# Performance work log

Hardware: AMD Instinct MI355X
Metric: run time of the kernel (lower is better)

The kernel has to match this reference:

```python
import jax, jax.numpy as jnp
import numpy as np

EMBED_DIM = 1024
NUM_HEADS = 16
HEAD_DIM = EMBED_DIM // NUM_HEADS
THRESHOLD = 0.001
B, S = 8, 1024


def setup_inputs() -> dict:
    key = jax.random.key(0)
    ks = jax.random.split(key, 7)
    sc = 1.0 / np.sqrt(EMBED_DIM)
    return {
        "x": jax.random.normal(ks[0], (B, S, EMBED_DIM), dtype=jnp.float32),
        "Wq": jax.random.normal(ks[1], (NUM_HEADS, EMBED_DIM, HEAD_DIM), dtype=jnp.float32) * sc,
        "bq": jax.random.normal(ks[2], (NUM_HEADS, HEAD_DIM), dtype=jnp.float32) * 0.01,
        "Wk": jax.random.normal(ks[3], (NUM_HEADS, EMBED_DIM, HEAD_DIM), dtype=jnp.float32) * sc,
        "bk": jax.random.normal(ks[4], (NUM_HEADS, HEAD_DIM), dtype=jnp.float32) * 0.01,
        "Wv": jax.random.normal(ks[5], (NUM_HEADS, EMBED_DIM, HEAD_DIM), dtype=jnp.float32) * sc,
        "bv": jax.random.normal(ks[6], (NUM_HEADS, HEAD_DIM), dtype=jnp.float32) * 0.01,
    }


def thresholded_softmax(scores, threshold):
    # softmax over last dim, zero entries below threshold, renormalize
    s = jax.nn.softmax(scores, axis=-1)
    s = jnp.where(s < threshold, 0.0, s)
    return s / (jnp.sum(s, axis=-1, keepdims=True) + 1e-12)


def reference(x, Wq, bq, Wk, bk, Wv, bv):
    # x: [B,S,D]; Wq/Wk/Wv: [H,D,e]; biases: [H,e]
    scale = jnp.asarray(EMBED_DIM ** 0.5, x.dtype)  # note: scales by sqrt(embed_dim), not head_dim
    Q = jnp.einsum("bsd,hde->hbse", x, Wq) + bq[:, None, None, :]
    K = jnp.einsum("bsd,hde->hbse", x, Wk) + bk[:, None, None, :]
    V = jnp.einsum("bsd,hde->hbse", x, Wv) + bv[:, None, None, :]
    scores = jnp.einsum("hbse,hbte->hbst", Q, K) / scale  # [H,B,S,S]
    att = thresholded_softmax(scores, THRESHOLD)
    latent = jnp.einsum("hbst,hbte->hbse", att, V)  # [H,B,S,e]
    # concat heads along last dim in head order -> [B,S,H*e]
    residual = jnp.transpose(latent, (1, 2, 0, 3)).reshape(x.shape[0], x.shape[1], -1)
    x_res = x + residual  # dropout p=0.0 -> identity
    return (x_res, att)
```

## Files before the change

### kernel.cpp

```cpp
#include <hip/hip_runtime.h>
#include <hip/hip_bf16.h>
#include <cstdint>
#include <cstddef>

#define B_ 8
#define S_ 1024
#define H_ 16
#define E_ 64
#define D_ 1024

typedef unsigned short u16;
typedef short s16x8 __attribute__((ext_vector_type(8)));
typedef float f32x4 __attribute__((ext_vector_type(4)));

__device__ __forceinline__ u16 f2b(float f) {
  union { float f; unsigned u; } v; v.f = f;
  unsigned u = v.u;
  return (u16)((u + 0x7FFFu + ((u >> 16) & 1u)) >> 16);
}

__device__ __forceinline__ void gload16(const void* g, void* lds) {
  __builtin_amdgcn_global_load_lds(
      (const __attribute__((address_space(1))) void*)g,
      (__attribute__((address_space(3))) void*)lds, 16, 0, 0);
}

#define BARL() do {                                          \
  asm volatile("s_waitcnt lgkmcnt(0)" ::: "memory");         \
  __builtin_amdgcn_sched_barrier(0);                         \
  __builtin_amdgcn_s_barrier();                              \
  __builtin_amdgcn_sched_barrier(0);                         \
  asm volatile("" ::: "memory");                             \
} while (0)

__global__ void k_prep(const float* __restrict__ x, u16* __restrict__ xb,
                       const float* __restrict__ Wq, const float* __restrict__ Wk,
                       const float* __restrict__ Wv, u16* __restrict__ wbt) {
  if (blockIdx.x < 4096) {
    size_t i = ((size_t)blockIdx.x * 256 + threadIdx.x) * 8;
    float4 a = *(const float4*)(x + i);
    float4 b = *(const float4*)(x + i + 4);
    uint4 o;
    o.x = f2b(a.x) | ((unsigned)f2b(a.y) << 16);
    o.y = f2b(a.z) | ((unsigned)f2b(a.w) << 16);
    o.z = f2b(b.x) | ((unsigned)f2b(b.y) << 16);
    o.w = f2b(b.z) | ((unsigned)f2b(b.w) << 16);
    *(uint4*)(xb + i) = o;
    return;
  }
  __shared__ u16 T[64][65];
  int bid = blockIdx.x - 4096;
  int d0 = (bid & 15) * 64;
  int mh = bid >> 4;
  int mat = mh >> 4, h = mh & 15;
  const float* W = (mat == 0) ? Wq : (mat == 1) ? Wk : Wv;
  int tid = threadIdx.x;
#pragma unroll
  for (int rep = 0; rep < 4; rep++) {
    int dl = rep * 16 + (tid >> 4);
    int e0 = (tid & 15) * 4;
    float4 v = *(const float4*)(W + (size_t)h * (D_ * E_) + (size_t)(d0 + dl) * E_ + e0);
    T[dl][e0] = f2b(v.x); T[dl][e0 + 1] = f2b(v.y);
    T[dl][e0 + 2] = f2b(v.z); T[dl][e0 + 3] = f2b(v.w);
  }
  __syncthreads();
#pragma unroll
  for (int rep = 0; rep < 4; rep++) {
    int el = rep * 16 + (tid >> 4);
    int dl0 = (tid & 15) * 4;
    ushort4 o;
    o.x = T[dl0][el]; o.y = T[dl0 + 1][el]; o.z = T[dl0 + 2][el]; o.w = T[dl0 + 3][el];
    int n = mat * 1024 + h * 64 + el;
    *(ushort4*)(wbt + (size_t)n * D_ + d0 + dl0) = o;
  }
}

__global__ __launch_bounds__(256) void k_qkv(
    const u16* __restrict__ xb, const u16* __restrict__ wbt,
    const float* __restrict__ bq, const float* __restrict__ bk, const float* __restrict__ bv,
    u16* __restrict__ Qb, u16* __restrict__ Kb, u16* __restrict__ Vt) {
  __shared__ u16 As[128 * 64];
  __shared__ u16 Bs[128 * 64];
  int tid = threadIdx.x, l = tid & 63, w = tid >> 6;
  int bid = blockIdx.x;
  int xcd = bid & 7, i = bid >> 3;
  int m0 = (xcd * 8 + i / 24) * 128;
  int n0 = (i % 24) * 128;
  int wm = w >> 1, wn = w & 1;
  int rl = l & 15, kg = l >> 4;
  f32x4 acc[4][4] = {};
  for (int k0 = 0; k0 < D_; k0 += 64) {
#pragma unroll
    for (int i2 = 0; i2 < 4; i2++) {
      int ci = w * 4 + i2;
      int r = ci * 8 + (l >> 3);
      int c = (l & 7) ^ (r & 7);
      gload16(xb  + (size_t)(m0 + r) * D_ + k0 + c * 8, (char*)As + ci * 1024);
      gload16(wbt + (size_t)(n0 + r) * D_ + k0 + c * 8, (char*)Bs + ci * 1024);
    }
    __syncthreads();
#pragma unroll
    for (int kk = 0; kk < 2; kk++) {
      s16x8 af[4], bfr[4];
      int chunk = kk * 4 + kg;
#pragma unroll
      for (int fm = 0; fm < 4; fm++) {
        int r = wm * 64 + fm * 16 + rl;
        af[fm] = *(const s16x8*)(As + r * 64 + ((chunk ^ (r & 7)) * 8));
      }
#pragma unroll
      for (int fn = 0; fn < 4; fn++) {
        int r = wn * 64 + fn * 16 + rl;
        bfr[fn] = *(const s16x8*)(Bs + r * 64 + ((chunk ^ (r & 7)) * 8));
      }
#pragma unroll
      for (int fm = 0; fm < 4; fm++)
#pragma unroll
        for (int fn = 0; fn < 4; fn++)
          acc[fm][fn] = __builtin_amdgcn_mfma_f32_16x16x32_bf16(af[fm], bfr[fn], acc[fm][fn], 0, 0, 0);
    }
    __syncthreads();
  }
#pragma unroll
  for (int fn = 0; fn < 4; fn++) {
    int n = n0 + wn * 64 + fn * 16 + rl;
    int mat = n >> 10, h = (n >> 6) & 15, e = n & 63;
    const float* bias = (mat == 0) ? bq : (mat == 1) ? bk : bv;
    float bval = bias[h * 64 + e];
    if (mat == 2) {
#pragma unroll
      for (int fm = 0; fm < 4; fm++) {
        int sq = m0 + wm * 64 + fm * 16 + kg * 4;
        int bb = sq >> 10, s = sq & 1023;
        ushort4 o;
        o.x = f2b(acc[fm][fn][0] + bval);
        o.y = f2b(acc[fm][fn][1] + bval);
        o.z = f2b(acc[fm][fn][2] + bval);
        o.w = f2b(acc[fm][fn][3] + bval);
        *(ushort4*)(Vt + ((size_t)((h * B_ + bb) * E_ + e) << 10) + s) = o;
      }
    } else {
      u16* dst = (mat == 0) ? Qb : Kb;
#pragma unroll
      for (int fm = 0; fm < 4; fm++)
#pragma unroll
        for (int j = 0; j < 4; j++) {
          int m = m0 + wm * 64 + fm * 16 + kg * 4 + j;
          int bb = m >> 10, s = m & 1023;
          dst[(size_t)((h * B_ + bb) * S_ + s) * E_ + e] = f2b(acc[fm][fn][j] + bval);
        }
    }
  }
}

__global__ __launch_bounds__(512, 2) void f_attn(
    const u16* __restrict__ Qb, const u16* __restrict__ Kb, const u16* __restrict__ Vt,
    const float* __restrict__ x, float* __restrict__ att, float* __restrict__ out) {
  __shared__ u16 Qlds[64 * 64];
  __shared__ u16 KV[1024 * 64];
  __shared__ u16 Ab[2][64 * 64];
  __shared__ float red[3][64][4];

  int p = blockIdx.x;
  int L = (p & 7) * 256 + (p >> 3);
  int hb = L >> 4, mblk = L & 15;
  int m0 = mblk * 64;
  int tid = threadIdx.x, l = tid & 63, w = tid >> 6;
  int rl = l & 15, kg = l >> 4;
  int rh = w >> 2, cq = w & 3;

  const u16* Qp = Qb + (size_t)hb * (S_ * E_) + (size_t)m0 * E_;
  const u16* Kp = Kb + (size_t)hb * (S_ * E_);
  const u16* Vp = Vt + (size_t)hb * (S_ * E_);

  {
    int r = w * 8 + (l >> 3), c = (l & 7) ^ (r & 7);
    gload16(Qp + (size_t)r * E_ + c * 8, (char*)Qlds + w * 1024);
  }
#pragma unroll
  for (int i = 0; i < 16; i++) {
    int ci = w * 16 + i;
    int r = ci * 8 + (l >> 3), c = (l & 7) ^ (r & 7);
    gload16(Kp + (size_t)r * E_ + c * 8, (char*)KV + ci * 1024);
  }
  __syncthreads();

  s16x8 af[2][2];
#pragma unroll
  for (int fm = 0; fm < 2; fm++)
#pragma unroll
    for (int kk = 0; kk < 2; kk++) {
      int r = rh * 32 + fm * 16 + rl, ch = kk * 4 + kg;
      af[fm][kk] = *(const s16x8*)((const char*)Qlds + r * 128 + ((ch ^ (r & 7)) * 16));
    }

  f32x4 acc[2][16];
#pragma unroll
  for (int fm = 0; fm < 2; fm++)
#pragma unroll
    for (int ct = 0; ct < 16; ct++)
#pragma unroll
      for (int j = 0; j < 4; j++) acc[fm][ct][j] = 0.f;

#pragma unroll
  for (int ct = 0; ct < 16; ct++) {
    s16x8 bf[2];
#pragma unroll
    for (int kk = 0; kk < 2; kk++) {
      int r = ct * 64 + cq * 16 + rl, ch = kk * 4 + kg;
      bf[kk] = *(const s16x8*)((const char*)KV + r * 128 + ((ch ^ (r & 7)) * 16));
    }
#pragma unroll
    for (int fm = 0; fm < 2; fm++)
#pragma unroll
      for (int kk = 0; kk < 2; kk++)
        acc[fm][ct] = __builtin_amdgcn_mfma_f32_16x16x32_bf16(af[fm][kk], bf[kk], acc[fm][ct], 0, 0, 0);
  }
  __syncthreads();

#pragma unroll
  for (int i = 0; i < 16; i++) {
    int ci = w * 16 + i;
    int e = ci >> 1, hf = ci & 1;
    int c = ((hf * 64 + l) & ~7) | ((l & 7) ^ (e & 7));
    gload16(Vp + (size_t)e * S_ + c * 8, (char*)KV + e * 2048 + hf * 1024);
  }

  float mx[2][4], Z[2][4], Z2[2][4];
#pragma unroll
  for (int fm = 0; fm < 2; fm++)
#pragma unroll
    for (int j = 0; j < 4; j++) {
      float m = acc[fm][0][j];
#pragma unroll
      for (int ct = 1; ct < 16; ct++) m = fmaxf(m, acc[fm][ct][j]);
#pragma unroll
      for (int off = 8; off >= 1; off >>= 1) m = fmaxf(m, __shfl_xor(m, off));
      mx[fm][j] = m;
    }
  if (rl == 0) {
#pragma unroll
    for (int fm = 0; fm < 2; fm++)
#pragma unroll
      for (int j = 0; j < 4; j++) red[0][rh * 32 + fm * 16 + kg * 4 + j][cq] = mx[fm][j];
  }
  BARL();
#pragma unroll
  for (int fm = 0; fm < 2; fm++)
#pragma unroll
    for (int j = 0; j < 4; j++) {
      f32x4 r4 = *(const f32x4*)&red[0][rh * 32 + fm * 16 + kg * 4 + j][0];
      mx[fm][j] = fmaxf(fmaxf(r4[0], r4[1]), fmaxf(r4[2], r4[3]));
    }
#pragma unroll
  for (int fm = 0; fm < 2; fm++)
#pragma unroll
    for (int j = 0; j < 4; j++) {
      float s = 0.f;
#pragma unroll
      for (int ct = 0; ct < 16; ct++) {
        float e = __expf((acc[fm][ct][j] - mx[fm][j]) * 0.03125f);
        acc[fm][ct][j] = e;
        s += e;
      }
#pragma unroll
      for (int off = 8; off >= 1; off >>= 1) s += __shfl_xor(s, off);
      Z[fm][j] = s;
    }
  if (rl == 0) {
#pragma unroll
    for (int fm = 0; fm < 2; fm++)
#pragma unroll
      for (int j = 0; j < 4; j++) red[1][rh * 32 + fm * 16 + kg * 4 + j][cq] = Z[fm][j];
  }
  BARL();
#pragma unroll
  for (int fm = 0; fm < 2; fm++)
#pragma unroll
    for (int j = 0; j < 4; j++) {
      f32x4 r4 = *(const f32x4*)&red[1][rh * 32 + fm * 16 + kg * 4 + j][0];
      Z[fm][j] = r4[0] + r4[1] + r4[2] + r4[3];
    }
#pragma unroll
  for (int fm = 0; fm < 2; fm++)
#pragma unroll
    for (int j = 0; j < 4; j++) {
      float thr = 0.001f * Z[fm][j];
      float s = 0.f;
#pragma unroll
      for (int ct = 0; ct < 16; ct++) {
        float e = acc[fm][ct][j];
        e = (e >= thr) ? e : 0.f;
        acc[fm][ct][j] = e;
        s += e;
      }
#pragma unroll
      for (int off = 8; off >= 1; off >>= 1) s += __shfl_xor(s, off);
      Z2[fm][j] = s;
    }
  if (rl == 0) {
#pragma unroll
    for (int fm = 0; fm < 2; fm++)
#pragma unroll
      for (int j = 0; j < 4; j++) red[2][rh * 32 + fm * 16 + kg * 4 + j][cq] = Z2[fm][j];
  }
  BARL();
#pragma unroll
  for (int fm = 0; fm < 2; fm++)
#pragma unroll
    for (int j = 0; j < 4; j++) {
      f32x4 r4 = *(const f32x4*)&red[2][rh * 32 + fm * 16 + kg * 4 + j][0];
      float z2 = r4[0] + r4[1] + r4[2] + r4[3];
      float inv = 1.f / (z2 + 1e-12f * Z[fm][j]);
#pragma unroll
      for (int ct = 0; ct < 16; ct++) acc[fm][ct][j] *= inv;
    }

  asm volatile("s_waitcnt vmcnt(0)" ::: "memory");
  __builtin_amdgcn_sched_barrier(0);

  float* attp = att + ((size_t)hb << 20) + ((size_t)m0 << 10);
#pragma unroll
  for (int fm = 0; fm < 2; fm++)
#pragma unroll
    for (int j = 0; j < 4; j++) {
      int m = rh * 32 + fm * 16 + kg * 4 + j;
#pragma unroll
      for (int ct = 0; ct < 16; ct++)
        attp[((size_t)m << 10) + ct * 64 + cq * 16 + rl] = acc[fm][ct][j];
    }

  int mh2 = w >> 1, nh2 = w & 1;
  f32x4 acc2[2];
#pragma unroll
  for (int fn = 0; fn < 2; fn++)
#pragma unroll
    for (int j = 0; j < 4; j++) acc2[fn][j] = 0.f;

#pragma unroll
  for (int fm = 0; fm < 2; fm++)
#pragma unroll
    for (int j = 0; j < 4; j++) {
      int m = rh * 32 + fm * 16 + kg * 4 + j;
      int tl = cq * 16 + rl;
      *(u16*)((char*)Ab[0] + m * 128 + (((tl >> 3) ^ (m & 7)) * 16) + (tl & 7) * 2)
          = f2b(acc[fm][0][j]);
    }
  BARL();

#pragma unroll
  for (int ct = 0; ct < 16; ct++) {
    s16x8 a2[2], b2[2][2];
#pragma unroll
    for (int kk = 0; kk < 2; kk++) {
      int ch = kk * 4 + kg;
      int rA = mh2 * 16 + rl;
      a2[kk] = *(const s16x8*)((const char*)Ab[ct & 1] + rA * 128 + ((ch ^ (rA & 7)) * 16));
#pragma unroll
      for (int fn = 0; fn < 2; fn++) {
        int e = nh2 * 32 + fn * 16 + rl;
        b2[fn][kk] = *(const s16x8*)((const char*)KV + e * 2048 + ct * 128 + ((ch ^ (e & 7)) * 16));
      }
    }
    if (ct < 15) {
#pragma unroll
      for (int fm = 0; fm < 2; fm++)
#pragma unroll
        for (int j = 0; j < 4; j++) {
          int m = rh * 32 + fm * 16 + kg * 4 + j;
          int tl = cq * 16 + rl;
          *(u16*)((char*)Ab[(ct + 1) & 1] + m * 128 + (((tl >> 3) ^ (m & 7)) * 16) + (tl & 7) * 2)
              = f2b(acc[fm][ct + 1][j]);
        }
    }
    __builtin_amdgcn_s_setprio(1);
#pragma unroll
    for (int fn = 0; fn < 2; fn++)
#pragma unroll
      for (int kk = 0; kk < 2; kk++)
        acc2[fn] = __builtin_amdgcn_mfma_f32_16x16x32_bf16(a2[kk], b2[fn][kk], acc2[fn], 0, 0, 0);
    __builtin_amdgcn_s_setprio(0);
    BARL();
  }

  int h = hb >> 3, bb = hb & 7;
#pragma unroll
  for (int fn = 0; fn < 2; fn++)
#pragma unroll
    for (int j = 0; j < 4; j++) {
      int m = m0 + mh2 * 16 + kg * 4 + j;
      int e = h * 64 + nh2 * 32 + fn * 16 + rl;
      size_t idx = (((size_t)bb * S_ + m) << 10) + e;
      out[idx] = x[idx] + acc2[fn][j];
    }
}

extern "C" void kernel_launch(void* const* d_in, const int* in_sizes, int n_in,
                              void* d_out, int out_size, void* d_ws, size_t ws_size,
                              hipStream_t stream) {
  const float* x  = (const float*)d_in[0];
  const float* Wq = (const float*)d_in[1];
  const float* bq = (const float*)d_in[2];
  const float* Wk = (const float*)d_in[3];
  const float* bk = (const float*)d_in[4];
  const float* Wv = (const float*)d_in[5];
  const float* bv = (const float*)d_in[6];
  float* xres = (float*)d_out;
  float* att  = xres + (size_t)B_ * S_ * D_;

  char* ws = (char*)d_ws;
  u16* xb  = (u16*)(ws);
  u16* wbt = (u16*)(ws + 16777216);
  u16* Qb  = (u16*)(ws + 23068672);
  u16* Kb  = (u16*)(ws + 39845888);
  u16* Vt  = (u16*)(ws + 56623104);

  k_prep  <<<dim3(4864), dim3(256), 0, stream>>>(x, xb, Wq, Wk, Wv, wbt);
  k_qkv   <<<dim3(1536), dim3(256), 0, stream>>>(xb, wbt, bq, bk, bv, Qb, Kb, Vt);
  f_attn  <<<dim3(2048), dim3(512), 0, stream>>>(Qb, Kb, Vt, x, att, xres);
}
```

Measured before the change: 296.7 us.

## Stream K and V through double-buffered LDS chunks with smaller 32-row attention blocks

The attention kernel now uses 32 query rows per block and 256 threads instead of 64 rows and 512 threads, and it stops holding the whole K or V tile in LDS. K and V are streamed in 128-key chunks through a double buffer, with the next chunk's async load issued while MFMAs run on the current one. The attention-matrix stores are interleaved with the PV loop, and the x residual is prefetched early. This shrinks LDS per block so more blocks can be resident and hides load latency. The cost is twice as many blocks, each re-reading K and V, plus extra barriers per chunk.

Result: slower. 447.9 us (+51.0%).

```diff
diff --git a/kernel.cpp b/kernel.cpp
--- a/kernel.cpp
+++ b/kernel.cpp
@@ -153,21 +153,20 @@
   }
 }
 
-__global__ __launch_bounds__(512, 2) void f_attn(
+__global__ __launch_bounds__(256) void f_attn(
     const u16* __restrict__ Qb, const u16* __restrict__ Kb, const u16* __restrict__ Vt,
     const float* __restrict__ x, float* __restrict__ att, float* __restrict__ out) {
-  __shared__ u16 Qlds[64 * 64];
-  __shared__ u16 KV[1024 * 64];
-  __shared__ u16 Ab[2][64 * 64];
-  __shared__ float red[3][64][4];
+  __shared__ u16 Kc[2][128 * 64];
+  __shared__ u16 Ab[2][32 * 128];
+  __shared__ u16 Qlds[32 * 64];
+  __shared__ float red[3][32][4];
 
   int p = blockIdx.x;
-  int L = (p & 7) * 256 + (p >> 3);
-  int hb = L >> 4, mblk = L & 15;
-  int m0 = mblk * 64;
+  int L = (p & 7) * 512 + (p >> 3);
+  int hb = L >> 5, mblk = L & 31;
+  int m0 = mblk * 32;
   int tid = threadIdx.x, l = tid & 63, w = tid >> 6;
   int rl = l & 15, kg = l >> 4;
-  int rh = w >> 2, cq = w & 3;
 
   const u16* Qp = Qb + (size_t)hb * (S_ * E_) + (size_t)m0 * E_;
   const u16* Kp = Kb + (size_t)hb * (S_ * E_);
@@ -178,10 +177,10 @@
     gload16(Qp + (size_t)r * E_ + c * 8, (char*)Qlds + w * 1024);
   }
 #pragma unroll
-  for (int i = 0; i < 16; i++) {
-    int ci = w * 16 + i;
+  for (int i = 0; i < 4; i++) {
+    int ci = w * 4 + i;
     int r = ci * 8 + (l >> 3), c = (l & 7) ^ (r & 7);
-    gload16(Kp + (size_t)r * E_ + c * 8, (char*)KV + ci * 1024);
+    gload16(Kp + (size_t)r * E_ + c * 8, (char*)Kc[0] + ci * 1024);
   }
   __syncthreads();
 
@@ -190,41 +189,66 @@
   for (int fm = 0; fm < 2; fm++)
 #pragma unroll
     for (int kk = 0; kk < 2; kk++) {
-      int r = rh * 32 + fm * 16 + rl, ch = kk * 4 + kg;
-      af[fm][kk] = *(const s16x8*)((const char*)Qlds + r * 128 + ((ch ^ (r & 7)) * 16));
+      int q = fm * 16 + rl, ch = kk * 4 + kg;
+      af[fm][kk] = *(const s16x8*)((const char*)Qlds + q * 128 + ((ch ^ (q & 7)) * 16));
     }
 
   f32x4 acc[2][16];
 #pragma unroll
   for (int fm = 0; fm < 2; fm++)
 #pragma unroll
-    for (int ct = 0; ct < 16; ct++)
-#pragma unroll
-      for (int j = 0; j < 4; j++) acc[fm][ct][j] = 0.f;
-
-#pragma unroll
-  for (int ct = 0; ct < 16; ct++) {
-    s16x8 bf[2];
-#pragma unroll
-    for (int kk = 0; kk < 2; kk++) {
-      int r = ct * 64 + cq * 16 + rl, ch = kk * 4 + kg;
-      bf[kk] = *(const s16x8*)((const char*)KV + r * 128 + ((ch ^ (r & 7)) * 16));
-    }
+    for (int tc = 0; tc < 16; tc++)
+#pragma unroll
+      for (int j = 0; j < 4; j++) acc[fm][tc][j] = 0.f;
+
+#pragma unroll
+  for (int c = 0; c < 8; c++) {
+    if (c < 7) {
+#pragma unroll
+      for (int i = 0; i < 4; i++) {
+        int ci = w * 4 + i;
+        int r = ci * 8 + (l >> 3), cc = (l & 7) ^ (r & 7);
+        gload16(Kp + (size_t)((c + 1) * 128 + r) * E_ + cc * 8,
+                (char*)Kc[(c + 1) & 1] + ci * 1024);
+      }
+    }
+    s16x8 bf[2][2];
+#pragma unroll
+    for (int fn = 0; fn < 2; fn++)
+#pragma unroll
+      for (int kk = 0; kk < 2; kk++) {
+        int r = w * 32 + fn * 16 + rl, ch = kk * 4 + kg;
+        bf[fn][kk] = *(const s16x8*)((const char*)Kc[c & 1] + r * 128 + ((ch ^ (r & 7)) * 16));
+      }
 #pragma unroll
     for (int fm = 0; fm < 2; fm++)
 #pragma unroll
-      for (int kk = 0; kk < 2; kk++)
-        acc[fm][ct] = __builtin_amdgcn_mfma_f32_16x16x32_bf16(af[fm][kk], bf[kk], acc[fm][ct], 0, 0, 0);
-  }
-  __syncthreads();
-
-#pragma unroll
-  for (int i = 0; i < 16; i++) {
-    int ci = w * 16 + i;
-    int e = ci >> 1, hf = ci & 1;
-    int c = ((hf * 64 + l) & ~7) | ((l & 7) ^ (e & 7));
-    gload16(Vp + (size_t)e * S_ + c * 8, (char*)KV + e * 2048 + hf * 1024);
-  }
+      for (int fn = 0; fn < 2; fn++)
+#pragma unroll
+        for (int kk = 0; kk < 2; kk++)
+          acc[fm][c * 2 + fn] = __builtin_amdgcn_mfma_f32_16x16x32_bf16(
+              af[fm][kk], bf[fn][kk], acc[fm][c * 2 + fn], 0, 0, 0);
+    __syncthreads();
+  }
+
+#pragma unroll
+  for (int i = 0; i < 4; i++) {
+    int ci = w * 4 + i;
+    int e = ci * 4 + (l >> 4);
+    int s = l & 15;
+    int cl = (s & 8) | ((s & 7) ^ (e & 7));
+    gload16(Vp + (size_t)e * S_ + cl * 8, (char*)Kc[0] + ci * 1024);
+  }
+  int h = hb >> 3, bb = hb & 7;
+  float xv[2][4];
+#pragma unroll
+  for (int fm = 0; fm < 2; fm++)
+#pragma unroll
+    for (int j = 0; j < 4; j++) {
+      int q = m0 + fm * 16 + kg * 4 + j;
+      int e = h * 64 + w * 16 + rl;
+      xv[fm][j] = x[(((size_t)bb * S_ + q) << 10) + e];
+    }
 
   float mx[2][4], Z[2][4], Z2[2][4];
 #pragma unroll
@@ -233,7 +257,7 @@
     for (int j = 0; j < 4; j++) {
       float m = acc[fm][0][j];
 #pragma unroll
-      for (int ct = 1; ct < 16; ct++) m = fmaxf(m, acc[fm][ct][j]);
+      for (int tc = 1; tc < 16; tc++) m = fmaxf(m, acc[fm][tc][j]);
 #pragma unroll
       for (int off = 8; off >= 1; off >>= 1) m = fmaxf(m, __shfl_xor(m, off));
       mx[fm][j] = m;
@@ -242,14 +266,14 @@
 #pragma unroll
     for (int fm = 0; fm < 2; fm++)
 #pragma unroll
-      for (int j = 0; j < 4; j++) red[0][rh * 32 + fm * 16 + kg * 4 + j][cq] = mx[fm][j];
+      for (int j = 0; j < 4; j++) red[0][fm * 16 + kg * 4 + j][w] = mx[fm][j];
   }
   BARL();
 #pragma unroll
   for (int fm = 0; fm < 2; fm++)
 #pragma unroll
     for (int j = 0; j < 4; j++) {
-      f32x4 r4 = *(const f32x4*)&red[0][rh * 32 + fm * 16 + kg * 4 + j][0];
+      f32x4 r4 = *(const f32x4*)&red[0][fm * 16 + kg * 4 + j][0];
       mx[fm][j] = fmaxf(fmaxf(r4[0], r4[1]), fmaxf(r4[2], r4[3]));
     }
 #pragma unroll
@@ -258,9 +282,9 @@
     for (int j = 0; j < 4; j++) {
       float s = 0.f;
 #pragma unroll
-      for (int ct = 0; ct < 16; ct++) {
-        float e = __expf((acc[fm][ct][j] - mx[fm][j]) * 0.03125f);
-        acc[fm][ct][j] = e;
+      for (int tc = 0; tc < 16; tc++) {
+        float e = __expf((acc[fm][tc][j] - mx[fm][j]) * 0.03125f);
+        acc[fm][tc][j] = e;
         s += e;
       }
 #pragma unroll
@@ -271,14 +295,14 @@
 #pragma unroll
     for (int fm = 0; fm < 2; fm++)
 #pragma unroll
-      for (int j = 0; j < 4; j++) red[1][rh * 32 + fm * 16 + kg * 4 + j][cq] = Z[fm][j];
+      for (int j = 0; j < 4; j++) red[1][fm * 16 + kg * 4 + j][w] = Z[fm][j];
   }
   BARL();
 #pragma unroll
   for (int fm = 0; fm < 2; fm++)
 #pragma unroll
     for (int j = 0; j < 4; j++) {
-      f32x4 r4 = *(const f32x4*)&red[1][rh * 32 + fm * 16 + kg * 4 + j][0];
+      f32x4 r4 = *(const f32x4*)&red[1][fm * 16 + kg * 4 + j][0];
       Z[fm][j] = r4[0] + r4[1] + r4[2] + r4[3];
     }
 #pragma unroll
@@ -288,10 +312,10 @@
       float thr = 0.001f * Z[fm][j];
       float s = 0.f;
 #pragma unroll
-      for (int ct = 0; ct < 16; ct++) {
-        float e = acc[fm][ct][j];
+      for (int tc = 0; tc < 16; tc++) {
+        float e = acc[fm][tc][j];
         e = (e >= thr) ? e : 0.f;
-        acc[fm][ct][j] = e;
+        acc[fm][tc][j] = e;
         s += e;
       }
 #pragma unroll
@@ -302,96 +326,101 @@
 #pragma unroll
     for (int fm = 0; fm < 2; fm++)
 #pragma unroll
-      for (int j = 0; j < 4; j++) red[2][rh * 32 + fm * 16 + kg * 4 + j][cq] = Z2[fm][j];
+      for (int j = 0; j < 4; j++) red[2][fm * 16 + kg * 4 + j][w] = Z2[fm][j];
   }
   BARL();
 #pragma unroll
   for (int fm = 0; fm < 2; fm++)
 #pragma unroll
     for (int j = 0; j < 4; j++) {
-      f32x4 r4 = *(const f32x4*)&red[2][rh * 32 + fm * 16 + kg * 4 + j][0];
+      f32x4 r4 = *(const f32x4*)&red[2][fm * 16 + kg * 4 + j][0];
       float z2 = r4[0] + r4[1] + r4[2] + r4[3];
       float inv = 1.f / (z2 + 1e-12f * Z[fm][j]);
 #pragma unroll
-      for (int ct = 0; ct < 16; ct++) acc[fm][ct][j] *= inv;
-    }
-
-  asm volatile("s_waitcnt vmcnt(0)" ::: "memory");
-  __builtin_amdgcn_sched_barrier(0);
-
+      for (int tc = 0; tc < 16; tc++) acc[fm][tc][j] *= inv;
+    }
+
+#pragma unroll
+  for (int fm = 0; fm < 2; fm++)
+#pragma unroll
+    for (int fn = 0; fn < 2; fn++)
+#pragma unroll
+      for (int j = 0; j < 4; j++) {
+        int q = fm * 16 + kg * 4 + j;
+        int tl = w * 32 + fn * 16 + rl;
+        int chk = tl >> 3;
+        int sw = (chk & 8) | ((chk & 7) ^ (q & 7));
+        *(u16*)((char*)Ab[0] + q * 256 + sw * 16 + (tl & 7) * 2) = f2b(acc[fm][fn][j]);
+      }
+  __syncthreads();
+
+  f32x4 acc2[2] = {};
   float* attp = att + ((size_t)hb << 20) + ((size_t)m0 << 10);
 #pragma unroll
-  for (int fm = 0; fm < 2; fm++)
-#pragma unroll
-    for (int j = 0; j < 4; j++) {
-      int m = rh * 32 + fm * 16 + kg * 4 + j;
-#pragma unroll
-      for (int ct = 0; ct < 16; ct++)
-        attp[((size_t)m << 10) + ct * 64 + cq * 16 + rl] = acc[fm][ct][j];
-    }
-
-  int mh2 = w >> 1, nh2 = w & 1;
-  f32x4 acc2[2];
-#pragma unroll
-  for (int fn = 0; fn < 2; fn++)
-#pragma unroll
-    for (int j = 0; j < 4; j++) acc2[fn][j] = 0.f;
-
-#pragma unroll
-  for (int fm = 0; fm < 2; fm++)
-#pragma unroll
-    for (int j = 0; j < 4; j++) {
-      int m = rh * 32 + fm * 16 + kg * 4 + j;
-      int tl = cq * 16 + rl;
-      *(u16*)((char*)Ab[0] + m * 128 + (((tl >> 3) ^ (m & 7)) * 16) + (tl & 7) * 2)
-          = f2b(acc[fm][0][j]);
-    }
-  BARL();
-
-#pragma unroll
-  for (int ct = 0; ct < 16; ct++) {
-    s16x8 a2[2], b2[2][2];
-#pragma unroll
-    for (int kk = 0; kk < 2; kk++) {
-      int ch = kk * 4 + kg;
-      int rA = mh2 * 16 + rl;
-      a2[kk] = *(const s16x8*)((const char*)Ab[ct & 1] + rA * 128 + ((ch ^ (rA & 7)) * 16));
-#pragma unroll
-      for (int fn = 0; fn < 2; fn++) {
-        int e = nh2 * 32 + fn * 16 + rl;
-        b2[fn][kk] = *(const s16x8*)((const char*)KV + e * 2048 + ct * 128 + ((ch ^ (e & 7)) * 16));
-      }
-    }
-    if (ct < 15) {
+  for (int c = 0; c < 8; c++) {
+    if (c < 7) {
+#pragma unroll
+      for (int i = 0; i < 4; i++) {
+        int ci = w * 4 + i;
+        int e = ci * 4 + (l >> 4);
+        int s = l & 15;
+        int cl = (s & 8) | ((s & 7) ^ (e & 7));
+        gload16(Vp + (size_t)e * S_ + (c + 1) * 128 + cl * 8,
+                (char*)Kc[(c + 1) & 1] + ci * 1024);
+      }
 #pragma unroll
       for (int fm = 0; fm < 2; fm++)
 #pragma unroll
+        for (int fn = 0; fn < 2; fn++)
+#pragma unroll
+          for (int j = 0; j < 4; j++) {
+            int q = fm * 16 + kg * 4 + j;
+            int tl = w * 32 + fn * 16 + rl;
+            int chk = tl >> 3;
+            int sw = (chk & 8) | ((chk & 7) ^ (q & 7));
+            *(u16*)((char*)Ab[(c + 1) & 1] + q * 256 + sw * 16 + (tl & 7) * 2)
+                = f2b(acc[fm][(c + 1) * 2 + fn][j]);
+          }
+    }
+#pragma unroll
+    for (int ks = 0; ks < 4; ks++) {
+      int chk = ks * 4 + kg;
+      s16x8 a2[2], b2;
+#pragma unroll
+      for (int fm = 0; fm < 2; fm++) {
+        int q = fm * 16 + rl;
+        int sw = (chk & 8) | ((chk & 7) ^ (q & 7));
+        a2[fm] = *(const s16x8*)((const char*)Ab[c & 1] + q * 256 + sw * 16);
+      }
+      {
+        int e = w * 16 + rl;
+        int sw = (chk & 8) | ((chk & 7) ^ (e & 7));
+        b2 = *(const s16x8*)((const char*)Kc[c & 1] + e * 256 + sw * 16);
+      }
+#pragma unroll
+      for (int fm = 0; fm < 2; fm++)
+        acc2[fm] = __builtin_amdgcn_mfma_f32_16x16x32_bf16(a2[fm], b2, acc2[fm], 0, 0, 0);
+    }
+#pragma unroll
+    for (int fm = 0; fm < 2; fm++)
+#pragma unroll
+      for (int fn = 0; fn < 2; fn++)
+#pragma unroll
         for (int j = 0; j < 4; j++) {
-          int m = rh * 32 + fm * 16 + kg * 4 + j;
-          int tl = cq * 16 + rl;
-          *(u16*)((char*)Ab[(ct + 1) & 1] + m * 128 + (((tl >> 3) ^ (m & 7)) * 16) + (tl & 7) * 2)
-              = f2b(acc[fm][ct + 1][j]);
+          int q = fm * 16 + kg * 4 + j;
+          int t = c * 128 + w * 32 + fn * 16 + rl;
+          attp[((size_t)q << 10) + t] = acc[fm][c * 2 + fn][j];
         }
-    }
-    __builtin_amdgcn_s_setprio(1);
-#pragma unroll
-    for (int fn = 0; fn < 2; fn++)
-#pragma unroll
-      for (int kk = 0; kk < 2; kk++)
-        acc2[fn] = __builtin_amdgcn_mfma_f32_16x16x32_bf16(a2[kk], b2[fn][kk], acc2[fn], 0, 0, 0);
-    __builtin_amdgcn_s_setprio(0);
-    BARL();
-  }
-
-  int h = hb >> 3, bb = hb & 7;
-#pragma unroll
-  for (int fn = 0; fn < 2; fn++)
-#pragma unroll
-    for (int j = 0; j < 4; j++) {
-      int m = m0 + mh2 * 16 + kg * 4 + j;
-      int e = h * 64 + nh2 * 32 + fn * 16 + rl;
-      size_t idx = (((size_t)bb * S_ + m) << 10) + e;
-      out[idx] = x[idx] + acc2[fn][j];
+    __syncthreads();
+  }
+
+#pragma unroll
+  for (int fm = 0; fm < 2; fm++)
+#pragma unroll
+    for (int j = 0; j < 4; j++) {
+      int q = m0 + fm * 16 + kg * 4 + j;
+      int e = h * 64 + w * 16 + rl;
+      out[(((size_t)bb * S_ + q) << 10) + e] = xv[fm][j] + acc2[fm][j];
     }
 }
 
@@ -417,5 +446,5 @@
 
   k_prep  <<<dim3(4864), dim3(256), 0, stream>>>(x, xb, Wq, Wk, Wv, wbt);
   k_qkv   <<<dim3(1536), dim3(256), 0, stream>>>(xb, wbt, bq, bk, bv, Qb, Kb, Vt);
-  f_attn  <<<dim3(2048), dim3(512), 0, stream>>>(Qb, Kb, Vt, x, att, xres);
-}
+  f_attn  <<<dim3(4096), dim3(256), 0, stream>>>(Qb, Kb, Vt, x, att, xres);
+}
```

## Transpose QK^T MFMA so each lane owns a query row, vectorize att stores

Applied to the files above, without the earlier changes.

The score MFMA is computed as K·Q^T so each lane holds one query row across 32 key tiles. Row max and sum reductions then need only two cross-lane shuffles instead of four per row. The attention matrix is stored with float4 writes instead of scalar writes. The P tiles for the PV matmul are packed with v_cvt_pk_bf16_f32 into 8-byte LDS stores. The aim is to cut reduction shuffles and store instruction count on a kernel dominated by writing the large att output, with a new LDS reduction layout and P-tile write pattern.

Result: slower. 316.5 us (+6.6%).

```diff
diff --git a/kernel.cpp b/kernel.cpp
--- a/kernel.cpp
+++ b/kernel.cpp
@@ -17,6 +17,12 @@
   union { float f; unsigned u; } v; v.f = f;
   unsigned u = v.u;
   return (u16)((u + 0x7FFFu + ((u >> 16) & 1u)) >> 16);
+}
+
+__device__ __forceinline__ unsigned cvtpk(float a, float b) {
+  unsigned r;
+  asm("v_cvt_pk_bf16_f32 %0, %1, %2" : "=v"(r) : "v"(a), "v"(b));
+  return r;
 }
 
 __device__ __forceinline__ void gload16(const void* g, void* lds) {
@@ -159,7 +165,7 @@
   __shared__ u16 Qlds[64 * 64];
   __shared__ u16 KV[1024 * 64];
   __shared__ u16 Ab[2][64 * 64];
-  __shared__ float red[3][64][4];
+  __shared__ float red[3][4][16][2];
 
   int p = blockIdx.x;
   int L = (p & 7) * 256 + (p >> 3);
@@ -167,7 +173,8 @@
   int m0 = mblk * 64;
   int tid = threadIdx.x, l = tid & 63, w = tid >> 6;
   int rl = l & 15, kg = l >> 4;
-  int rh = w >> 2, cq = w & 3;
+  int qg = w >> 1, pr = w & 1;
+  int q = qg * 16 + rl;
 
   const u16* Qp = Qb + (size_t)hb * (S_ * E_) + (size_t)m0 * E_;
   const u16* Kp = Kb + (size_t)hb * (S_ * E_);
@@ -185,36 +192,23 @@
   }
   __syncthreads();
 
-  s16x8 af[2][2];
-#pragma unroll
-  for (int fm = 0; fm < 2; fm++)
-#pragma unroll
-    for (int kk = 0; kk < 2; kk++) {
-      int r = rh * 32 + fm * 16 + rl, ch = kk * 4 + kg;
-      af[fm][kk] = *(const s16x8*)((const char*)Qlds + r * 128 + ((ch ^ (r & 7)) * 16));
-    }
-
-  f32x4 acc[2][16];
-#pragma unroll
-  for (int fm = 0; fm < 2; fm++)
-#pragma unroll
-    for (int ct = 0; ct < 16; ct++)
-#pragma unroll
-      for (int j = 0; j < 4; j++) acc[fm][ct][j] = 0.f;
-
-#pragma unroll
-  for (int ct = 0; ct < 16; ct++) {
-    s16x8 bf[2];
-#pragma unroll
-    for (int kk = 0; kk < 2; kk++) {
-      int r = ct * 64 + cq * 16 + rl, ch = kk * 4 + kg;
-      bf[kk] = *(const s16x8*)((const char*)KV + r * 128 + ((ch ^ (r & 7)) * 16));
-    }
-#pragma unroll
-    for (int fm = 0; fm < 2; fm++)
-#pragma unroll
-      for (int kk = 0; kk < 2; kk++)
-        acc[fm][ct] = __builtin_amdgcn_mfma_f32_16x16x32_bf16(af[fm][kk], bf[kk], acc[fm][ct], 0, 0, 0);
+  s16x8 qf[2];
+#pragma unroll
+  for (int kk = 0; kk < 2; kk++)
+    qf[kk] = *(const s16x8*)((const char*)Qlds + q * 128 + (((kk * 4 + kg) ^ (q & 7)) * 16));
+
+  f32x4 acc[32];
+#pragma unroll
+  for (int i = 0; i < 32; i++)
+#pragma unroll
+    for (int j = 0; j < 4; j++) acc[i][j] = 0.f;
+#pragma unroll
+  for (int i = 0; i < 32; i++) {
+    int tr = (2 * i + pr) * 16 + rl;
+    s16x8 kf0 = *(const s16x8*)((const char*)KV + tr * 128 + ((kg ^ (tr & 7)) * 16));
+    s16x8 kf1 = *(const s16x8*)((const char*)KV + tr * 128 + (((4 + kg) ^ (tr & 7)) * 16));
+    acc[i] = __builtin_amdgcn_mfma_f32_16x16x32_bf16(kf0, qf[0], acc[i], 0, 0, 0);
+    acc[i] = __builtin_amdgcn_mfma_f32_16x16x32_bf16(kf1, qf[1], acc[i], 0, 0, 0);
   }
   __syncthreads();
 
@@ -226,153 +220,106 @@
     gload16(Vp + (size_t)e * S_ + c * 8, (char*)KV + e * 2048 + hf * 1024);
   }
 
-  float mx[2][4], Z[2][4], Z2[2][4];
-#pragma unroll
-  for (int fm = 0; fm < 2; fm++)
-#pragma unroll
-    for (int j = 0; j < 4; j++) {
-      float m = acc[fm][0][j];
-#pragma unroll
-      for (int ct = 1; ct < 16; ct++) m = fmaxf(m, acc[fm][ct][j]);
-#pragma unroll
-      for (int off = 8; off >= 1; off >>= 1) m = fmaxf(m, __shfl_xor(m, off));
-      mx[fm][j] = m;
-    }
-  if (rl == 0) {
-#pragma unroll
-    for (int fm = 0; fm < 2; fm++)
-#pragma unroll
-      for (int j = 0; j < 4; j++) red[0][rh * 32 + fm * 16 + kg * 4 + j][cq] = mx[fm][j];
+  float m, Z, Z2;
+  {
+    float mm = acc[0][0];
+#pragma unroll
+    for (int i = 0; i < 32; i++)
+#pragma unroll
+      for (int j = 0; j < 4; j++) mm = fmaxf(mm, acc[i][j]);
+    mm = fmaxf(mm, __shfl_xor(mm, 16));
+    mm = fmaxf(mm, __shfl_xor(mm, 32));
+    if (kg == 0) red[0][qg][rl][pr] = mm;
   }
   BARL();
-#pragma unroll
-  for (int fm = 0; fm < 2; fm++)
-#pragma unroll
-    for (int j = 0; j < 4; j++) {
-      f32x4 r4 = *(const f32x4*)&red[0][rh * 32 + fm * 16 + kg * 4 + j][0];
-      mx[fm][j] = fmaxf(fmaxf(r4[0], r4[1]), fmaxf(r4[2], r4[3]));
-    }
-#pragma unroll
-  for (int fm = 0; fm < 2; fm++)
-#pragma unroll
-    for (int j = 0; j < 4; j++) {
-      float s = 0.f;
-#pragma unroll
-      for (int ct = 0; ct < 16; ct++) {
-        float e = __expf((acc[fm][ct][j] - mx[fm][j]) * 0.03125f);
-        acc[fm][ct][j] = e;
+  m = fmaxf(red[0][qg][rl][0], red[0][qg][rl][1]);
+  {
+    float s = 0.f;
+#pragma unroll
+    for (int i = 0; i < 32; i++)
+#pragma unroll
+      for (int j = 0; j < 4; j++) {
+        float e = __expf((acc[i][j] - m) * 0.03125f);
+        acc[i][j] = e;
         s += e;
       }
-#pragma unroll
-      for (int off = 8; off >= 1; off >>= 1) s += __shfl_xor(s, off);
-      Z[fm][j] = s;
-    }
-  if (rl == 0) {
-#pragma unroll
-    for (int fm = 0; fm < 2; fm++)
-#pragma unroll
-      for (int j = 0; j < 4; j++) red[1][rh * 32 + fm * 16 + kg * 4 + j][cq] = Z[fm][j];
+    s += __shfl_xor(s, 16);
+    s += __shfl_xor(s, 32);
+    if (kg == 0) red[1][qg][rl][pr] = s;
   }
   BARL();
-#pragma unroll
-  for (int fm = 0; fm < 2; fm++)
-#pragma unroll
-    for (int j = 0; j < 4; j++) {
-      f32x4 r4 = *(const f32x4*)&red[1][rh * 32 + fm * 16 + kg * 4 + j][0];
-      Z[fm][j] = r4[0] + r4[1] + r4[2] + r4[3];
-    }
-#pragma unroll
-  for (int fm = 0; fm < 2; fm++)
-#pragma unroll
-    for (int j = 0; j < 4; j++) {
-      float thr = 0.001f * Z[fm][j];
-      float s = 0.f;
-#pragma unroll
-      for (int ct = 0; ct < 16; ct++) {
-        float e = acc[fm][ct][j];
+  Z = red[1][qg][rl][0] + red[1][qg][rl][1];
+  {
+    float thr = 0.001f * Z;
+    float s = 0.f;
+#pragma unroll
+    for (int i = 0; i < 32; i++)
+#pragma unroll
+      for (int j = 0; j < 4; j++) {
+        float e = acc[i][j];
         e = (e >= thr) ? e : 0.f;
-        acc[fm][ct][j] = e;
+        acc[i][j] = e;
         s += e;
       }
-#pragma unroll
-      for (int off = 8; off >= 1; off >>= 1) s += __shfl_xor(s, off);
-      Z2[fm][j] = s;
-    }
-  if (rl == 0) {
-#pragma unroll
-    for (int fm = 0; fm < 2; fm++)
-#pragma unroll
-      for (int j = 0; j < 4; j++) red[2][rh * 32 + fm * 16 + kg * 4 + j][cq] = Z2[fm][j];
+    s += __shfl_xor(s, 16);
+    s += __shfl_xor(s, 32);
+    if (kg == 0) red[2][qg][rl][pr] = s;
   }
   BARL();
-#pragma unroll
-  for (int fm = 0; fm < 2; fm++)
-#pragma unroll
-    for (int j = 0; j < 4; j++) {
-      f32x4 r4 = *(const f32x4*)&red[2][rh * 32 + fm * 16 + kg * 4 + j][0];
-      float z2 = r4[0] + r4[1] + r4[2] + r4[3];
-      float inv = 1.f / (z2 + 1e-12f * Z[fm][j]);
-#pragma unroll
-      for (int ct = 0; ct < 16; ct++) acc[fm][ct][j] *= inv;
-    }
+  Z2 = red[2][qg][rl][0] + red[2][qg][rl][1];
+  {
+    float inv = 1.f / (Z2 + 1e-12f * Z);
+#pragma unroll
+    for (int i = 0; i < 32; i++)
+#pragma unroll
+      for (int j = 0; j < 4; j++) acc[i][j] *= inv;
+  }
 
   asm volatile("s_waitcnt vmcnt(0)" ::: "memory");
   __builtin_amdgcn_sched_barrier(0);
 
   float* attp = att + ((size_t)hb << 20) + ((size_t)m0 << 10);
 #pragma unroll
-  for (int fm = 0; fm < 2; fm++)
-#pragma unroll
-    for (int j = 0; j < 4; j++) {
-      int m = rh * 32 + fm * 16 + kg * 4 + j;
-#pragma unroll
-      for (int ct = 0; ct < 16; ct++)
-        attp[((size_t)m << 10) + ct * 64 + cq * 16 + rl] = acc[fm][ct][j];
-    }
-
-  int mh2 = w >> 1, nh2 = w & 1;
+  for (int i = 0; i < 32; i++) {
+    int t = (2 * i + pr) * 16 + kg * 4;
+    *(float4*)(attp + ((size_t)q << 10) + t) = *(float4*)&acc[i];
+  }
+
+#define PUBLISH(BUF, C) do {                                                     \
+    _Pragma("unroll")                                                            \
+    for (int ii = 0; ii < 2; ii++) {                                             \
+      int ai = (C) * 2 + ii;                                                     \
+      uint2 pk;                                                                  \
+      pk.x = cvtpk(acc[ai][0], acc[ai][1]);                                      \
+      pk.y = cvtpk(acc[ai][2], acc[ai][3]);                                      \
+      int cc = (pr + 2 * ii) * 2 + (kg >> 1);                                    \
+      *(uint2*)((char*)(BUF) + q * 128 + ((cc ^ (q & 7)) * 16) + (kg & 1) * 8) = pk; \
+    }                                                                            \
+  } while (0)
+
   f32x4 acc2[2];
 #pragma unroll
   for (int fn = 0; fn < 2; fn++)
 #pragma unroll
     for (int j = 0; j < 4; j++) acc2[fn][j] = 0.f;
 
-#pragma unroll
-  for (int fm = 0; fm < 2; fm++)
-#pragma unroll
-    for (int j = 0; j < 4; j++) {
-      int m = rh * 32 + fm * 16 + kg * 4 + j;
-      int tl = cq * 16 + rl;
-      *(u16*)((char*)Ab[0] + m * 128 + (((tl >> 3) ^ (m & 7)) * 16) + (tl & 7) * 2)
-          = f2b(acc[fm][0][j]);
-    }
+  PUBLISH(Ab[0], 0);
   BARL();
 
 #pragma unroll
-  for (int ct = 0; ct < 16; ct++) {
+  for (int c = 0; c < 16; c++) {
     s16x8 a2[2], b2[2][2];
 #pragma unroll
     for (int kk = 0; kk < 2; kk++) {
       int ch = kk * 4 + kg;
-      int rA = mh2 * 16 + rl;
-      a2[kk] = *(const s16x8*)((const char*)Ab[ct & 1] + rA * 128 + ((ch ^ (rA & 7)) * 16));
+      a2[kk] = *(const s16x8*)((const char*)Ab[c & 1] + q * 128 + ((ch ^ (q & 7)) * 16));
 #pragma unroll
       for (int fn = 0; fn < 2; fn++) {
-        int e = nh2 * 32 + fn * 16 + rl;
-        b2[fn][kk] = *(const s16x8*)((const char*)KV + e * 2048 + ct * 128 + ((ch ^ (e & 7)) * 16));
-      }
-    }
-    if (ct < 15) {
-#pragma unroll
-      for (int fm = 0; fm < 2; fm++)
-#pragma unroll
-        for (int j = 0; j < 4; j++) {
-          int m = rh * 32 + fm * 16 + kg * 4 + j;
-          int tl = cq * 16 + rl;
-          *(u16*)((char*)Ab[(ct + 1) & 1] + m * 128 + (((tl >> 3) ^ (m & 7)) * 16) + (tl & 7) * 2)
-              = f2b(acc[fm][ct + 1][j]);
-        }
-    }
+        int e = pr * 32 + fn * 16 + rl;
+        b2[fn][kk] = *(const s16x8*)((const char*)KV + e * 2048 + c * 128 + ((ch ^ (e & 7)) * 16));
+      }
+    }
+    if (c < 15) PUBLISH(Ab[(c + 1) & 1], c + 1);
     __builtin_amdgcn_s_setprio(1);
 #pragma unroll
     for (int fn = 0; fn < 2; fn++)
@@ -388,9 +335,9 @@
   for (int fn = 0; fn < 2; fn++)
 #pragma unroll
     for (int j = 0; j < 4; j++) {
-      int m = m0 + mh2 * 16 + kg * 4 + j;
-      int e = h * 64 + nh2 * 32 + fn * 16 + rl;
-      size_t idx = (((size_t)bb * S_ + m) << 10) + e;
+      int mq = m0 + qg * 16 + kg * 4 + j;
+      int e = h * 64 + pr * 32 + fn * 16 + rl;
+      size_t idx = (((size_t)bb * S_ + mq) << 10) + e;
       out[idx] = x[idx] + acc2[fn][j];
     }
 }
```
